# Kernel tuning notes

Hardware: AMD Instinct MI355X
Metric: run time of the kernel (lower is better)

## Reference

```python
import jax, jax.numpy as jnp
import numpy as np

C = 512
NUM_HEADS = 8


def setup_inputs() -> dict:
    key = jax.random.key(0)
    ks = jax.random.split(key, 9)
    s = 1.0 / np.sqrt(C)
    inp = {
        "x": jax.random.normal(ks[0], (2, C, 64, 64), dtype=jnp.float32),
        "Wq": jax.random.uniform(ks[1], (C, C), jnp.float32, -s, s),
        "bq": jax.random.uniform(ks[2], (C,), jnp.float32, -s, s),
        "Wk": jax.random.uniform(ks[3], (C, C), jnp.float32, -s, s),
        "bk": jax.random.uniform(ks[4], (C,), jnp.float32, -s, s),
        "Wv": jax.random.uniform(ks[5], (C, C), jnp.float32, -s, s),
        "bv": jax.random.uniform(ks[6], (C,), jnp.float32, -s, s),
        "Wp": jax.random.uniform(ks[7], (C, C), jnp.float32, -s, s),
        "bp": jax.random.uniform(ks[8], (C,), jnp.float32, -s, s),
    }
    return inp


def _split_heads(t):
    # [B, S, C] -> [B, h, S, d]
    B, S, Ct = t.shape
    return t.reshape(B, S, NUM_HEADS, Ct // NUM_HEADS).transpose(0, 2, 1, 3)


def reference(x, Wq, bq, Wk, bk, Wv, bv, Wp, bp):
    B, Ct, H, W = x.shape
    tok = x.transpose(0, 2, 3, 1).reshape(B, H * W, Ct)  # [B, S, C]
    q = _split_heads(tok @ Wq.T + bq)
    k = _split_heads(tok @ Wk.T + bk)
    v = _split_heads(tok @ Wv.T + bv)
    d = q.shape[-1]
    scores = jnp.einsum("bhsd,bhtd->bhst", q, k) / jnp.sqrt(jnp.float32(d))
    attn = jax.nn.softmax(scores, axis=-1)
    out = jnp.einsum("bhst,bhtd->bhsd", attn, v)
    out = out.transpose(0, 2, 1, 3).reshape(B, H * W, Ct)  # merge heads
    out = out @ Wp.T + bp
    return out.reshape(B, H, W, Ct).transpose(0, 3, 1, 2)
```

## Files before the change

kernel.cpp:

```cpp
#include <hip/hip_runtime.h>
#include <stdint.h>
#include <math.h>

typedef unsigned short u16;
typedef uint32_t u32;
typedef short bf16x8 __attribute__((ext_vector_type(8)));
typedef float f32x4  __attribute__((ext_vector_type(4)));

#define DEV __device__ __forceinline__

DEV u16 f2bf(float f) {
    union { float f; u32 u; } x; x.f = f;
    u32 lsb = (x.u >> 16) & 1u;
    x.u += 0x7fffu + lsb;
    return (u16)(x.u >> 16);
}

DEV u32 pack2(float a, float b) {
    union { float f; u32 u; } x, y; x.f = a; y.f = b;
    return __builtin_amdgcn_perm(y.u + 0x8000u, x.u + 0x8000u, 0x07060302u);
}

#if __has_builtin(__builtin_amdgcn_exp2f)
DEV float fexp2(float x) { return __builtin_amdgcn_exp2f(x); }
#else
DEV float fexp2(float x) { return __expf(x * 0.69314718056f); }
#endif

DEV f32x4 mfma16(bf16x8 a, bf16x8 b, f32x4 c) {
    return __builtin_amdgcn_mfma_f32_16x16x32_bf16(a, b, c, 0, 0, 0);
}

__global__ __launch_bounds__(256) void prep_kernel(const float* __restrict__ x,
                                                   u16* __restrict__ tok,
                                                   const float* __restrict__ w0,
                                                   const float* __restrict__ w1,
                                                   const float* __restrict__ w2,
                                                   const float* __restrict__ w3,
                                                   u16* __restrict__ dst) {
    __shared__ u16 t[64][65];
    const int id = blockIdx.x, tid = threadIdx.x;
    if (id < 1024) {
        const int b = id >> 9, c0 = ((id >> 6) & 7) * 64, s0 = (id & 63) * 64;
        const float* xb = x + ((size_t)b * 512 + c0) * 4096 + s0;
        u16* tb = tok + ((size_t)b * 4096 + s0) * 512 + c0;
        {
            const int jc = tid & 15, i0 = tid >> 4;
#pragma unroll
            for (int ii = 0; ii < 4; ii++) {
                int i = i0 * 4 + ii;
                float4 v = *(const float4*)&xb[(size_t)i * 4096 + jc * 4];
                t[i][jc * 4 + 0] = f2bf(v.x);
                t[i][jc * 4 + 1] = f2bf(v.y);
                t[i][jc * 4 + 2] = f2bf(v.z);
                t[i][jc * 4 + 3] = f2bf(v.w);
            }
        }
        __syncthreads();
        {
            const int j = tid & 31, i0 = tid >> 5;
#pragma unroll
            for (int ii = 0; ii < 8; ii++) {
                int srow = i0 * 8 + ii;
                u32 v = (u32)t[j * 2][srow] | ((u32)t[j * 2 + 1][srow] << 16);
                *(u32*)(&tb[(size_t)srow * 512 + j * 2]) = v;
            }
        }
    } else {
        const int id2 = id - 1024;
        const int j = id2 >> 8;
        const float* src = (j == 0) ? w0 : (j == 1) ? w1 : (j == 2) ? w2 : w3;
        int idx = ((id2 & 255) * 256 + tid) * 4;
        float4 v = *(const float4*)&src[idx];
        uint2 pv;
        pv.x = pack2(v.x, v.y);
        pv.y = pack2(v.z, v.w);
        *(uint2*)&dst[(size_t)j * 262144 + idx] = pv;
    }
}

DEV void proj_core(const u16* __restrict__ W, const float* __restrict__ bias,
                   const u16* __restrict__ Bb, void* __restrict__ out,
                   int b, int mode, float scale,
                   u16 (*__restrict__ Alds)[4096], u16 (*__restrict__ Blds)[4096]) {
    const int tid = threadIdx.x;
    const int wave = tid >> 6, lane = tid & 63, q = lane >> 4, c = lane & 15;
    const int m0 = blockIdx.y * 128, n0 = blockIdx.x * 128;

    const int cs = tid & 15, qs = (tid >> 4) & 3, ms = (tid >> 6) & 3;
    const u16* Asrc0 = W  + (size_t)(m0 + ms * 16 + cs) * 512 + qs * 8;
    const u16* Asrc1 = W  + (size_t)(m0 + (ms + 4) * 16 + cs) * 512 + qs * 8;
    const u16* Bsrc0 = Bb + (size_t)(n0 + ms * 16 + cs) * 512 + qs * 8;
    const u16* Bsrc1 = Bb + (size_t)(n0 + (ms + 4) * 16 + cs) * 512 + qs * 8;

    f32x4 acc[4][4] = {};

    int4 pa0 = *(const int4*)&Asrc0[0];
    int4 pa1 = *(const int4*)&Asrc1[0];
    int4 pb0 = *(const int4*)&Bsrc0[0];
    int4 pb1 = *(const int4*)&Bsrc1[0];
    int4 ha0 = *(const int4*)&Asrc0[32];
    int4 ha1 = *(const int4*)&Asrc1[32];
    int4 hb0 = *(const int4*)&Bsrc0[32];
    int4 hb1 = *(const int4*)&Bsrc1[32];
    *(int4*)&Alds[0][tid * 8]         = pa0;
    *(int4*)&Alds[0][(tid + 256) * 8] = pa1;
    *(int4*)&Blds[0][tid * 8]         = pb0;
    *(int4*)&Blds[0][(tid + 256) * 8] = pb1;
    __syncthreads();

    int p = 0, pw = 1;
    for (int it = 0; it < 16; it++) {
        const int kn = ((it + 2) & 15) * 32;

        int4 na0 = *(const int4*)&Asrc0[kn];
        int4 na1 = *(const int4*)&Asrc1[kn];
        int4 nb0 = *(const int4*)&Bsrc0[kn];
        int4 nb1 = *(const int4*)&Bsrc1[kn];

        bf16x8 af[4], bfr[4];
#pragma unroll
        for (int t = 0; t < 4; t++) {
            int gm = (((wave & 1) * 4 + t) * 4 + q) * 16 + c;
            af[t] = *(const bf16x8*)&Alds[p][gm * 8];
            int gn = (((wave >> 1) * 4 + t) * 4 + q) * 16 + c;
            bfr[t] = *(const bf16x8*)&Blds[p][gn * 8];
        }
#pragma unroll
        for (int mt = 0; mt < 4; mt++)
#pragma unroll
            for (int nt = 0; nt < 4; nt++)
                acc[mt][nt] = mfma16(af[mt], bfr[nt], acc[mt][nt]);

        *(int4*)&Alds[pw][tid * 8]         = ha0;
        *(int4*)&Alds[pw][(tid + 256) * 8] = ha1;
        *(int4*)&Blds[pw][tid * 8]         = hb0;
        *(int4*)&Blds[pw][(tid + 256) * 8] = hb1;
        ha0 = na0; ha1 = na1; hb0 = nb0; hb1 = nb1;
        __syncthreads();
        p = pw; pw = (pw == 2) ? 0 : pw + 1;
    }

    const int mbase = m0 + (wave & 1) * 64, nbase = n0 + (wave >> 1) * 64;
#pragma unroll
    for (int mt = 0; mt < 4; mt++) {
        int co0 = mbase + mt * 16 + q * 4;
        float b0 = bias[co0 + 0], b1 = bias[co0 + 1];
        float b2 = bias[co0 + 2], b3 = bias[co0 + 3];
#pragma unroll
        for (int nt = 0; nt < 4; nt++) {
            int scol = nbase + nt * 16 + c;
            float v0 = (acc[mt][nt][0] + b0) * scale;
            float v1 = (acc[mt][nt][1] + b1) * scale;
            float v2 = (acc[mt][nt][2] + b2) * scale;
            float v3 = (acc[mt][nt][3] + b3) * scale;
            if (mode == 0) {
                uint2 pv; pv.x = pack2(v0, v1); pv.y = pack2(v2, v3);
                size_t idx = ((size_t)(b * 8 + (co0 >> 6)) * 4096 + scol) * 64 + (co0 & 63);
                *(uint2*)&((u16*)out)[idx] = pv;
            } else if (mode == 1) {
                u16* o = (u16*)out;
                o[((size_t)(b * 512 + co0 + 0)) * 4096 + scol] = f2bf(v0);
                o[((size_t)(b * 512 + co0 + 1)) * 4096 + scol] = f2bf(v1);
                o[((size_t)(b * 512 + co0 + 2)) * 4096 + scol] = f2bf(v2);
                o[((size_t)(b * 512 + co0 + 3)) * 4096 + scol] = f2bf(v3);
            } else {
                float* o = (float*)out;
                o[((size_t)(b * 512 + co0 + 0)) * 4096 + scol] = v0;
                o[((size_t)(b * 512 + co0 + 1)) * 4096 + scol] = v1;
                o[((size_t)(b * 512 + co0 + 2)) * 4096 + scol] = v2;
                o[((size_t)(b * 512 + co0 + 3)) * 4096 + scol] = v3;
            }
        }
    }
}

__global__ __launch_bounds__(256) void qkv_kernel(const u16* __restrict__ Wbf,
                                                  const float* __restrict__ bq,
                                                  const float* __restrict__ bk,
                                                  const float* __restrict__ bv,
                                                  const u16* __restrict__ tok,
                                                  u16* __restrict__ Qb,
                                                  u16* __restrict__ Kb,
                                                  u16* __restrict__ Vb) {
    __shared__ u16 Alds[3][4096];
    __shared__ u16 Blds[3][4096];
    const int z = blockIdx.z, j = z >> 1, b = z & 1;
    const u16* W = Wbf + (size_t)j * 262144;
    const float* bias = (j == 0) ? bq : (j == 1) ? bk : bv;
    void* out = (j == 0) ? (void*)Qb : (j == 1) ? (void*)Kb : (void*)Vb;
    const float scale = (j == 0) ? 0.1803368801f : 1.0f;
    const int mode = (j == 2) ? 1 : 0;
    proj_core(W, bias, tok + (size_t)b * (4096 * 512), out, b, mode, scale, Alds, Blds);
}

__global__ __launch_bounds__(256) void projp_kernel(const u16* __restrict__ Wp,
                                                    const float* __restrict__ bp,
                                                    const u16* __restrict__ attout,
                                                    float* __restrict__ out) {
    __shared__ u16 Alds[3][4096];
    __shared__ u16 Blds[3][4096];
    const int b = blockIdx.z;
    proj_core(Wp, bp, attout + (size_t)b * (4096 * 512), out, b, 2, 1.0f, Alds, Blds);
}

__global__ __launch_bounds__(256) void attn_kernel(const u16* __restrict__ Qm,
                                                   const u16* __restrict__ Km,
                                                   const u16* __restrict__ Vm,
                                                   u16* __restrict__ attout) {
    __shared__ u16 Klds[2][4096];
    __shared__ u16 Vlds[2][4096];
    __shared__ u16 Plds[128 * 72];
    const int tid = threadIdx.x, wave = tid >> 6, lane = tid & 63;
    const int q = lane >> 4, c = lane & 15;
    const int bhd = blockIdx.y, s0 = blockIdx.x * 128;
    const u16* Qb = Qm + (size_t)bhd * (4096 * 64);
    const u16* Kb = Km + (size_t)bhd * (4096 * 64);
    const u16* Vb = Vm + (size_t)bhd * (64 * 4096);

    bf16x8 qf[2][2];
#pragma unroll
    for (int st = 0; st < 2; st++)
#pragma unroll
        for (int kd = 0; kd < 2; kd++)
            qf[st][kd] = *(const bf16x8*)
                &Qb[(size_t)(s0 + wave * 32 + st * 16 + c) * 64 + kd * 32 + q * 8];

    const int rr = tid & 15, qq = (tid >> 4) & 3, kk = (tid >> 6) & 1;
    const int t40 = tid >> 7, t41 = t40 + 2;
    const u16* Ksrc0 = Kb + (size_t)(t40 * 16 + rr) * 64 + kk * 32 + qq * 8;
    const u16* Ksrc1 = Kb + (size_t)(t41 * 16 + rr) * 64 + kk * 32 + qq * 8;
    const u16* Vsrc0 = Vb + (size_t)(t40 * 16 + rr) * 4096 + kk * 32 + qq * 8;
    const u16* Vsrc1 = Vb + (size_t)(t41 * 16 + rr) * 4096 + kk * 32 + qq * 8;
    u16* Prow = &Plds[(size_t)(wave * 32 + c) * 72];

    f32x4 oacc[4][2] = {};
    float lsum[2] = {0.f, 0.f};

    *(int4*)&Klds[0][tid * 8]         = *(const int4*)&Ksrc0[0];
    *(int4*)&Klds[0][(tid + 256) * 8] = *(const int4*)&Ksrc1[0];
    *(int4*)&Vlds[0][tid * 8]         = *(const int4*)&Vsrc0[0];
    *(int4*)&Vlds[0][(tid + 256) * 8] = *(const int4*)&Vsrc1[0];
    __syncthreads();

    for (int it = 0; it < 64; it++) {
        const int p = it & 1;
        const size_t t0n = (size_t)(((it + 1) & 63) * 64);

        int4 kst0 = *(const int4*)&Ksrc0[t0n * 64];
        int4 kst1 = *(const int4*)&Ksrc1[t0n * 64];
        int4 vst0 = *(const int4*)&Vsrc0[t0n];
        int4 vst1 = *(const int4*)&Vsrc1[t0n];

        f32x4 sacc[4][2] = {};
#pragma unroll
        for (int kd = 0; kd < 2; kd++) {
            bf16x8 ka[4];
#pragma unroll
            for (int tt = 0; tt < 4; tt++)
                ka[tt] = *(const bf16x8*)&Klds[p][(((tt * 2 + kd) * 4 + q) * 16 + c) * 8];
#pragma unroll
            for (int tt = 0; tt < 4; tt++)
#pragma unroll
                for (int st = 0; st < 2; st++)
                    sacc[tt][st] = mfma16(ka[tt], qf[st][kd], sacc[tt][st]);
        }

#pragma unroll
        for (int st = 0; st < 2; st++) {
#pragma unroll
            for (int tt = 0; tt < 4; tt++) {
                float p0 = fexp2(sacc[tt][st][0]);
                float p1 = fexp2(sacc[tt][st][1]);
                float p2 = fexp2(sacc[tt][st][2]);
                float p3 = fexp2(sacc[tt][st][3]);
                lsum[st] += (p0 + p1) + (p2 + p3);
                uint2 pv; pv.x = pack2(p0, p1); pv.y = pack2(p2, p3);
                *(uint2*)&Prow[st * (16 * 72) + tt * 16 + q * 4] = pv;
            }
        }

#pragma unroll
        for (int kt = 0; kt < 2; kt++) {
            bf16x8 va[4], pb[2];
#pragma unroll
            for (int dt = 0; dt < 4; dt++)
                va[dt] = *(const bf16x8*)&Vlds[p][(((dt * 2 + kt) * 4 + q) * 16 + c) * 8];
#pragma unroll
            for (int st = 0; st < 2; st++)
                pb[st] = *(const bf16x8*)&Prow[st * (16 * 72) + kt * 32 + q * 8];
#pragma unroll
            for (int dt = 0; dt < 4; dt++)
#pragma unroll
                for (int st = 0; st < 2; st++)
                    oacc[dt][st] = mfma16(va[dt], pb[st], oacc[dt][st]);
        }

        *(int4*)&Klds[1 - p][tid * 8]         = kst0;
        *(int4*)&Klds[1 - p][(tid + 256) * 8] = kst1;
        *(int4*)&Vlds[1 - p][tid * 8]         = vst0;
        *(int4*)&Vlds[1 - p][(tid + 256) * 8] = vst1;
        __syncthreads();
    }

    const int b = bhd >> 3, hd = bhd & 7;
#pragma unroll
    for (int st = 0; st < 2; st++) {
        float l = lsum[st];
        l += __shfl_xor(l, 16, 64);
        l += __shfl_xor(l, 32, 64);
        float rl = 1.0f / l;
        int s = s0 + wave * 32 + st * 16 + c;
#pragma unroll
        for (int dt = 0; dt < 4; dt++) {
            uint2 pv;
            pv.x = pack2(oacc[dt][st][0] * rl, oacc[dt][st][1] * rl);
            pv.y = pack2(oacc[dt][st][2] * rl, oacc[dt][st][3] * rl);
            size_t idx = ((size_t)(b * 4096 + s)) * 512 + hd * 64 + dt * 16 + q * 4;
            *(uint2*)&attout[idx] = pv;
        }
    }
}

extern "C" void kernel_launch(void* const* d_in, const int* in_sizes, int n_in,
                              void* d_out, int out_size, void* d_ws, size_t ws_size,
                              hipStream_t stream) {
    (void)in_sizes; (void)n_in; (void)out_size; (void)ws_size;
    const float* x  = (const float*)d_in[0];
    const float* Wq = (const float*)d_in[1];
    const float* bq = (const float*)d_in[2];
    const float* Wk = (const float*)d_in[3];
    const float* bk = (const float*)d_in[4];
    const float* Wv = (const float*)d_in[5];
    const float* bv = (const float*)d_in[6];
    const float* Wp = (const float*)d_in[7];
    const float* bp = (const float*)d_in[8];
    float* out = (float*)d_out;

    const size_t NTOK = (size_t)4 * 1024 * 1024;
    u16* tok = (u16*)d_ws;
    u16* Qb  = tok + NTOK;
    u16* Kb  = Qb + NTOK;
    u16* Vb  = Kb + NTOK;
    u16* Wbf = Vb + NTOK;
    u16* attout = tok;

    prep_kernel<<<dim3(2048), 256, 0, stream>>>(x, tok, Wq, Wk, Wv, Wp, Wbf);
    qkv_kernel<<<dim3(32, 4, 6), 256, 0, stream>>>(Wbf, bq, bk, bv, tok, Qb, Kb, Vb);
    attn_kernel<<<dim3(32, 16), 256, 0, stream>>>(Qb, Kb, Vb, attout);
    projp_kernel<<<dim3(32, 4, 2), 256, 0, stream>>>(Wbf + 3 * 262144, bp, attout, out);
}
```

Baseline: 224.1 us.

## Software-pipeline attention: overlap P·V of previous tile with QK and exp of current

Measured after the change: 224.7 us. Within noise of the previous version (+0.3%).

```diff
diff --git a/kernel.cpp b/kernel.cpp
--- a/kernel.cpp
+++ b/kernel.cpp
@@ -209,8 +209,8 @@
                                                    const u16* __restrict__ Vm,
                                                    u16* __restrict__ attout) {
     __shared__ u16 Klds[2][4096];
-    __shared__ u16 Vlds[2][4096];
-    __shared__ u16 Plds[128 * 72];
+    __shared__ u16 Vlds[3][4096];
+    __shared__ u16 Plds[2][8192];
     const int tid = threadIdx.x, wave = tid >> 6, lane = tid & 63;
     const int q = lane >> 4, c = lane & 15;
     const int bhd = blockIdx.y, s0 = blockIdx.x * 128;
@@ -232,7 +232,9 @@
     const u16* Ksrc1 = Kb + (size_t)(t41 * 16 + rr) * 64 + kk * 32 + qq * 8;
     const u16* Vsrc0 = Vb + (size_t)(t40 * 16 + rr) * 4096 + kk * 32 + qq * 8;
     const u16* Vsrc1 = Vb + (size_t)(t41 * 16 + rr) * 4096 + kk * 32 + qq * 8;
-    u16* Prow = &Plds[(size_t)(wave * 32 + c) * 72];
+
+    u16* Pwr       = &Plds[0][wave * 2048 + (q >> 1) * 128 + (q & 1) * 4 + c * 8];
+    const u16* Prd = &Plds[0][wave * 2048 + q * 128 + c * 8];
 
     f32x4 oacc[4][2] = {};
     float lsum[2] = {0.f, 0.f};
@@ -241,10 +243,20 @@
     *(int4*)&Klds[0][(tid + 256) * 8] = *(const int4*)&Ksrc1[0];
     *(int4*)&Vlds[0][tid * 8]         = *(const int4*)&Vsrc0[0];
     *(int4*)&Vlds[0][(tid + 256) * 8] = *(const int4*)&Vsrc1[0];
+    {
+        int4 z = {0, 0, 0, 0};
+        *(int4*)&Plds[1][tid * 8]         = z;
+        *(int4*)&Plds[1][(tid + 256) * 8] = z;
+        *(int4*)&Plds[1][(tid + 512) * 8] = z;
+        *(int4*)&Plds[1][(tid + 768) * 8] = z;
+        *(int4*)&Vlds[2][tid * 8]         = z;
+        *(int4*)&Vlds[2][(tid + 256) * 8] = z;
+    }
     __syncthreads();
 
+    int prv = 2, nxt = 1;
     for (int it = 0; it < 64; it++) {
-        const int p = it & 1;
+        const int pk = it & 1;
         const size_t t0n = (size_t)(((it + 1) & 63) * 64);
 
         int4 kst0 = *(const int4*)&Ksrc0[t0n * 64];
@@ -258,7 +270,7 @@
             bf16x8 ka[4];
 #pragma unroll
             for (int tt = 0; tt < 4; tt++)
-                ka[tt] = *(const bf16x8*)&Klds[p][(((tt * 2 + kd) * 4 + q) * 16 + c) * 8];
+                ka[tt] = *(const bf16x8*)&Klds[pk][(((tt * 2 + kd) * 4 + q) * 16 + c) * 8];
 #pragma unroll
             for (int tt = 0; tt < 4; tt++)
 #pragma unroll
@@ -266,41 +278,68 @@
                     sacc[tt][st] = mfma16(ka[tt], qf[st][kd], sacc[tt][st]);
         }
 
-#pragma unroll
-        for (int st = 0; st < 2; st++) {
-#pragma unroll
-            for (int tt = 0; tt < 4; tt++) {
-                float p0 = fexp2(sacc[tt][st][0]);
-                float p1 = fexp2(sacc[tt][st][1]);
-                float p2 = fexp2(sacc[tt][st][2]);
-                float p3 = fexp2(sacc[tt][st][3]);
-                lsum[st] += (p0 + p1) + (p2 + p3);
-                uint2 pv; pv.x = pack2(p0, p1); pv.y = pack2(p2, p3);
-                *(uint2*)&Prow[st * (16 * 72) + tt * 16 + q * 4] = pv;
-            }
-        }
-
+        {
+            const u16* Pp = Prd + (1 - pk) * 8192;
+#pragma unroll
+            for (int kt = 0; kt < 2; kt++) {
+                bf16x8 va[4], pb[2];
+#pragma unroll
+                for (int dt = 0; dt < 4; dt++)
+                    va[dt] = *(const bf16x8*)&Vlds[prv][(((dt * 2 + kt) * 4 + q) * 16 + c) * 8];
+#pragma unroll
+                for (int st = 0; st < 2; st++)
+                    pb[st] = *(const bf16x8*)&Pp[st * 1024 + kt * 512];
+#pragma unroll
+                for (int dt = 0; dt < 4; dt++)
+#pragma unroll
+                    for (int st = 0; st < 2; st++)
+                        oacc[dt][st] = mfma16(va[dt], pb[st], oacc[dt][st]);
+            }
+        }
+
+        {
+            u16* Pw = Pwr + pk * 8192;
+#pragma unroll
+            for (int st = 0; st < 2; st++) {
+#pragma unroll
+                for (int tt = 0; tt < 4; tt++) {
+                    float p0 = fexp2(sacc[tt][st][0]);
+                    float p1 = fexp2(sacc[tt][st][1]);
+                    float p2 = fexp2(sacc[tt][st][2]);
+                    float p3 = fexp2(sacc[tt][st][3]);
+                    lsum[st] += (p0 + p1) + (p2 + p3);
+                    uint2 pv; pv.x = pack2(p0, p1); pv.y = pack2(p2, p3);
+                    *(uint2*)&Pw[st * 1024 + tt * 256] = pv;
+                }
+            }
+        }
+
+        *(int4*)&Klds[1 - pk][tid * 8]         = kst0;
+        *(int4*)&Klds[1 - pk][(tid + 256) * 8] = kst1;
+        *(int4*)&Vlds[nxt][tid * 8]            = vst0;
+        *(int4*)&Vlds[nxt][(tid + 256) * 8]    = vst1;
+        __syncthreads();
+        prv = (prv == 2) ? 0 : prv + 1;
+        nxt = (nxt == 2) ? 0 : nxt + 1;
+    }
+
+    {
+        const u16* Pp = Prd + 8192;
 #pragma unroll
         for (int kt = 0; kt < 2; kt++) {
             bf16x8 va[4], pb[2];
 #pragma unroll
             for (int dt = 0; dt < 4; dt++)
-                va[dt] = *(const bf16x8*)&Vlds[p][(((dt * 2 + kt) * 4 + q) * 16 + c) * 8];
+                va[dt] = *(const bf16x8*)&Vlds[0][(((dt * 2 + kt) * 4 + q) * 16 + c) * 8];
 #pragma unroll
             for (int st = 0; st < 2; st++)
-                pb[st] = *(const bf16x8*)&Prow[st * (16 * 72) + kt * 32 + q * 8];
+                pb[st] = *(const bf16x8*)&Pp[st * 1024 + kt * 512];
 #pragma unroll
             for (int dt = 0; dt < 4; dt++)
 #pragma unroll
                 for (int st = 0; st < 2; st++)
                     oacc[dt][st] = mfma16(va[dt], pb[st], oacc[dt][st]);
         }
-
-        *(int4*)&Klds[1 - p][tid * 8]         = kst0;
-        *(int4*)&Klds[1 - p][(tid + 256) * 8] = kst1;
-        *(int4*)&Vlds[1 - p][tid * 8]         = vst0;
-        *(int4*)&Vlds[1 - p][(tid + 256) * 8] = vst1;
-        __syncthreads();
     }
 
     const int b = bhd >> 3, hd = bhd & 7;
```

## Split attention over key dimension with partial outputs and merge kernel

Applied to the files above, without the earlier changes.

After: 222.8 us. No clear change (-0.6%).

```diff
diff --git a/kernel.cpp b/kernel.cpp
--- a/kernel.cpp
+++ b/kernel.cpp
@@ -204,16 +204,18 @@
     proj_core(Wp, bp, attout + (size_t)b * (4096 * 512), out, b, 2, 1.0f, Alds, Blds);
 }
 
-__global__ __launch_bounds__(256) void attn_kernel(const u16* __restrict__ Qm,
-                                                   const u16* __restrict__ Km,
-                                                   const u16* __restrict__ Vm,
-                                                   u16* __restrict__ attout) {
+__global__ __launch_bounds__(256, 4) void attn_kernel(const u16* __restrict__ Qm,
+                                                      const u16* __restrict__ Km,
+                                                      const u16* __restrict__ Vm,
+                                                      float* __restrict__ Opart,
+                                                      float* __restrict__ Lpart) {
     __shared__ u16 Klds[2][4096];
     __shared__ u16 Vlds[2][4096];
-    __shared__ u16 Plds[128 * 72];
+    __shared__ u16 Plds[4][1024];
     const int tid = threadIdx.x, wave = tid >> 6, lane = tid & 63;
     const int q = lane >> 4, c = lane & 15;
-    const int bhd = blockIdx.y, s0 = blockIdx.x * 128;
+    const int bhd = blockIdx.y, s0 = blockIdx.x * 128, z = blockIdx.z;
+    const int tbase = z * 2048;
     const u16* Qb = Qm + (size_t)bhd * (4096 * 64);
     const u16* Kb = Km + (size_t)bhd * (4096 * 64);
     const u16* Vb = Vm + (size_t)bhd * (64 * 4096);
@@ -228,11 +230,13 @@
 
     const int rr = tid & 15, qq = (tid >> 4) & 3, kk = (tid >> 6) & 1;
     const int t40 = tid >> 7, t41 = t40 + 2;
-    const u16* Ksrc0 = Kb + (size_t)(t40 * 16 + rr) * 64 + kk * 32 + qq * 8;
-    const u16* Ksrc1 = Kb + (size_t)(t41 * 16 + rr) * 64 + kk * 32 + qq * 8;
-    const u16* Vsrc0 = Vb + (size_t)(t40 * 16 + rr) * 4096 + kk * 32 + qq * 8;
-    const u16* Vsrc1 = Vb + (size_t)(t41 * 16 + rr) * 4096 + kk * 32 + qq * 8;
-    u16* Prow = &Plds[(size_t)(wave * 32 + c) * 72];
+    const u16* Ksrc0 = Kb + (size_t)(tbase + t40 * 16 + rr) * 64 + kk * 32 + qq * 8;
+    const u16* Ksrc1 = Kb + (size_t)(tbase + t41 * 16 + rr) * 64 + kk * 32 + qq * 8;
+    const u16* Vsrc0 = Vb + (size_t)(t40 * 16 + rr) * 4096 + tbase + kk * 32 + qq * 8;
+    const u16* Vsrc1 = Vb + (size_t)(t41 * 16 + rr) * 4096 + tbase + kk * 32 + qq * 8;
+
+    u16* Pwr       = &Plds[wave][(q >> 1) * 128 + (q & 1) * 4 + c * 8];
+    const u16* Prd = &Plds[wave][q * 128 + c * 8];
 
     f32x4 oacc[4][2] = {};
     float lsum[2] = {0.f, 0.f};
@@ -243,9 +247,9 @@
     *(int4*)&Vlds[0][(tid + 256) * 8] = *(const int4*)&Vsrc1[0];
     __syncthreads();
 
-    for (int it = 0; it < 64; it++) {
+    for (int it = 0; it < 32; it++) {
         const int p = it & 1;
-        const size_t t0n = (size_t)(((it + 1) & 63) * 64);
+        const size_t t0n = (size_t)(((it + 1) & 31) * 64);
 
         int4 kst0 = *(const int4*)&Ksrc0[t0n * 64];
         int4 kst1 = *(const int4*)&Ksrc1[t0n * 64];
@@ -276,24 +280,19 @@
                 float p3 = fexp2(sacc[tt][st][3]);
                 lsum[st] += (p0 + p1) + (p2 + p3);
                 uint2 pv; pv.x = pack2(p0, p1); pv.y = pack2(p2, p3);
-                *(uint2*)&Prow[st * (16 * 72) + tt * 16 + q * 4] = pv;
-            }
-        }
-
-#pragma unroll
-        for (int kt = 0; kt < 2; kt++) {
-            bf16x8 va[4], pb[2];
-#pragma unroll
-            for (int dt = 0; dt < 4; dt++)
-                va[dt] = *(const bf16x8*)&Vlds[p][(((dt * 2 + kt) * 4 + q) * 16 + c) * 8];
-#pragma unroll
-            for (int st = 0; st < 2; st++)
-                pb[st] = *(const bf16x8*)&Prow[st * (16 * 72) + kt * 32 + q * 8];
-#pragma unroll
-            for (int dt = 0; dt < 4; dt++)
-#pragma unroll
-                for (int st = 0; st < 2; st++)
-                    oacc[dt][st] = mfma16(va[dt], pb[st], oacc[dt][st]);
+                *(uint2*)&Pwr[tt * 256] = pv;
+            }
+#pragma unroll
+            for (int kt = 0; kt < 2; kt++) {
+                bf16x8 va[4];
+#pragma unroll
+                for (int dt = 0; dt < 4; dt++)
+                    va[dt] = *(const bf16x8*)&Vlds[p][(((dt * 2 + kt) * 4 + q) * 16 + c) * 8];
+                bf16x8 pb = *(const bf16x8*)&Prd[kt * 512];
+#pragma unroll
+                for (int dt = 0; dt < 4; dt++)
+                    oacc[dt][st] = mfma16(va[dt], pb, oacc[dt][st]);
+            }
         }
 
         *(int4*)&Klds[1 - p][tid * 8]         = kst0;
@@ -303,23 +302,43 @@
         __syncthreads();
     }
 
-    const int b = bhd >> 3, hd = bhd & 7;
 #pragma unroll
     for (int st = 0; st < 2; st++) {
         float l = lsum[st];
         l += __shfl_xor(l, 16, 64);
         l += __shfl_xor(l, 32, 64);
-        float rl = 1.0f / l;
-        int s = s0 + wave * 32 + st * 16 + c;
+        const int s = s0 + wave * 32 + st * 16 + c;
+        const size_t rowbase = ((size_t)(z * 16 + bhd) * 4096 + s) * 64;
 #pragma unroll
         for (int dt = 0; dt < 4; dt++) {
-            uint2 pv;
-            pv.x = pack2(oacc[dt][st][0] * rl, oacc[dt][st][1] * rl);
-            pv.y = pack2(oacc[dt][st][2] * rl, oacc[dt][st][3] * rl);
-            size_t idx = ((size_t)(b * 4096 + s)) * 512 + hd * 64 + dt * 16 + q * 4;
-            *(uint2*)&attout[idx] = pv;
-        }
-    }
+            float4 ov;
+            ov.x = oacc[dt][st][0];
+            ov.y = oacc[dt][st][1];
+            ov.z = oacc[dt][st][2];
+            ov.w = oacc[dt][st][3];
+            *(float4*)&Opart[rowbase + dt * 16 + q * 4] = ov;
+        }
+        if (lane < 16)
+            Lpart[(size_t)z * 65536 + bhd * 4096 + s0 + wave * 32 + st * 16 + lane] = l;
+    }
+}
+
+__global__ __launch_bounds__(256) void merge_kernel(const float* __restrict__ Opart,
+                                                    const float* __restrict__ Lpart,
+                                                    u16* __restrict__ attout) {
+    const int i = blockIdx.x * 256 + threadIdx.x;
+    const int flat = i * 4;
+    const int row = flat >> 6, dv = flat & 63;
+    const int bhd = row >> 12, s = row & 4095;
+    const float l = Lpart[row] + Lpart[65536 + row];
+    const float rl = 1.0f / l;
+    const float4 a  = *(const float4*)&Opart[flat];
+    const float4 b4 = *(const float4*)&Opart[4194304 + flat];
+    uint2 pv;
+    pv.x = pack2((a.x + b4.x) * rl, (a.y + b4.y) * rl);
+    pv.y = pack2((a.z + b4.z) * rl, (a.w + b4.w) * rl);
+    const int b = bhd >> 3, hd = bhd & 7;
+    *(uint2*)&attout[((size_t)(b * 4096 + s)) * 512 + hd * 64 + dv] = pv;
 }
 
 extern "C" void kernel_launch(void* const* d_in, const int* in_sizes, int n_in,
@@ -344,9 +363,12 @@
     u16* Vb  = Kb + NTOK;
     u16* Wbf = Vb + NTOK;
     u16* attout = tok;
+    float* Opart = (float*)(Wbf + 4 * 262144);
+    float* Lpart = Opart + (size_t)2 * 4194304;
 
     prep_kernel<<<dim3(2048), 256, 0, stream>>>(x, tok, Wq, Wk, Wv, Wp, Wbf);
     qkv_kernel<<<dim3(32, 4, 6), 256, 0, stream>>>(Wbf, bq, bk, bv, tok, Qb, Kb, Vb);
-    attn_kernel<<<dim3(32, 16), 256, 0, stream>>>(Qb, Kb, Vb, attout);
+    attn_kernel<<<dim3(32, 16, 2), 256, 0, stream>>>(Qb, Kb, Vb, Opart, Lpart);
+    merge_kernel<<<dim3(4096), 256, 0, stream>>>(Opart, Lpart, attout);
     projp_kernel<<<dim3(32, 4, 2), 256, 0, stream>>>(Wbf + 3 * 262144, bp, attout, out);
 }
```
